# Kernel tuning notes

Hardware: AMD Instinct MI355X
Metric: run time of the kernel (lower is better)

## Reference

```python
import jax, jax.numpy as jnp
import numpy as np

B_SZ, L, D_MODEL = 2, 2048, 2048
INTER, HEADS, P, N, G, K = 4096, 64, 64, 128, 1, 4
CONV_DIM = INTER + 2 * G * N
EPS = 1e-5


def silu(x):
    return x * jax.nn.sigmoid(x)


def softplus_thresh(x, threshold=10.0):
    # matches source: where(x < thr, log(1+exp(x)), x)
    return jnp.where(x < threshold, jnp.log1p(jnp.exp(jnp.minimum(x, threshold))), x)


def setup_inputs() -> dict:
    key = jax.random.key(0)
    ks = jax.random.split(key, 8)
    s = 0.02
    return {
        "hidden_states": jax.random.normal(ks[0], (B_SZ, L, D_MODEL), jnp.float32),
        "W_z": jax.random.normal(ks[1], (D_MODEL, INTER), jnp.float32) * s,
        "W_xBC": jax.random.normal(ks[2], (D_MODEL, CONV_DIM), jnp.float32) * s,
        "W_dt": jax.random.normal(ks[3], (D_MODEL, HEADS), jnp.float32) * s,
        "conv_w": jax.random.normal(ks[4], (CONV_DIM, K), jnp.float32) * 0.1,
        "conv_b": jnp.zeros((CONV_DIM,), jnp.float32),
        "dt_bias": jax.random.uniform(ks[5], (HEADS,), jnp.float32, -2.0, 0.0),
        "A_log": jnp.log(jnp.arange(1, HEADS + 1, dtype=jnp.float32)),
        "D": jnp.ones((HEADS,), jnp.float32),
        "norm_w": jnp.ones((INTER,), jnp.float32),
        "W_out": jax.random.normal(ks[6], (INTER, D_MODEL), jnp.float32) * s,
    }


def reference(hidden_states, W_z, W_xBC, W_dt, conv_w, conv_b, dt_bias, A_log, D, norm_w, W_out):
    b, l, _ = hidden_states.shape
    Hg = HEADS // G  # heads per group

    gate = hidden_states @ W_z                      # [b,l,INTER]
    xBC = hidden_states @ W_xBC                     # [b,l,CONV_DIM]
    dt = softplus_thresh(hidden_states @ W_dt + dt_bias)  # [b,l,H]

    # causal depthwise conv1d + silu (padding=K-1, truncated to seq_len)
    xp = jnp.pad(xBC, ((0, 0), (K - 1, 0), (0, 0)))
    kern = jnp.transpose(conv_w)[:, None, :]        # [K,1,CONV_DIM] (WIO)
    xBC = jax.lax.conv_general_dilated(
        xp, kern, (1,), 'VALID',
        dimension_numbers=('NWC', 'WIO', 'NWC'),
        feature_group_count=CONV_DIM)
    xBC = silu(xBC + conv_b)

    gns = G * N
    x = xBC[..., :INTER].reshape(b, l, G, Hg, P)
    Bm = xBC[..., INTER:INTER + gns].reshape(b, l, G, N)
    Cm = xBC[..., INTER + gns:].reshape(b, l, G, N)

    A = -jnp.exp(A_log)                             # [H]
    dA = jnp.exp(dt * A).reshape(b, l, G, Hg)       # [b,l,G,Hg]
    dtx = dt.reshape(b, l, G, Hg)[..., None] * x    # [b,l,G,Hg,P]

    def step(state, inp):
        dA_t, dtx_t, B_t, C_t = inp
        # state: [b,G,Hg,P,N]
        state = state * dA_t[..., None, None] + dtx_t[..., None] * B_t[:, :, None, None, :]
        y_t = jnp.einsum('bghpn,bgn->bghp', state, C_t)
        return state, y_t

    xs = (jnp.moveaxis(dA, 1, 0), jnp.moveaxis(dtx, 1, 0),
          jnp.moveaxis(Bm, 1, 0), jnp.moveaxis(Cm, 1, 0))
    state0 = jnp.zeros((b, G, Hg, P, N), jnp.float32)
    _, ys = jax.lax.scan(step, state0, xs)          # [l,b,G,Hg,P]
    y = jnp.moveaxis(ys, 0, 1) + D.reshape(G, Hg)[..., None] * x
    scan_out = y.reshape(b, l, INTER)

    # gated RMSNorm within groups
    hs = scan_out.reshape(b, l, G, INTER // G).astype(jnp.float32)
    gt = gate.reshape(b, l, G, INTER // G).astype(jnp.float32)
    hs = hs * silu(gt)
    var = jnp.mean(hs * hs, axis=-1, keepdims=True)
    hs = hs * jax.lax.rsqrt(var + EPS)
    normed = norm_w * hs.reshape(b, l, INTER)

    return normed @ W_out
```

## Files before the change

kernel.cpp:

```cpp
#include <hip/hip_runtime.h>
#include <hip/hip_bf16.h>
#include <math.h>

typedef unsigned short u16;
typedef unsigned int   u32;
typedef __attribute__((ext_vector_type(8))) short short8;
typedef __attribute__((ext_vector_type(4))) float f32x4;

#define B_SZ     2
#define LSEQ     2048
#define DMODEL   2048
#define INTER    4096
#define HEADS    64
#define NSTATE   128
#define CONV_DIM 4352
#define XSTR     8576
#define NMAIN    8192
#define NTAILC   512
#define NTAILS   384
#define EPS      1e-5f
#define QCH      64
#define NCHUNK   (LSEQ / QCH)

__device__ __forceinline__ float bf2f(u16 u) {
    u32 v = ((u32)u) << 16;
    return __builtin_bit_cast(float, v);
}
__device__ __forceinline__ u16 f2bf(float x) {
    __hip_bfloat16 h = __float2bfloat16(x);
    return __builtin_bit_cast(u16, h);
}
__device__ __forceinline__ u32 pack2(float lo, float hi) {
    return (u32)f2bf(lo) | ((u32)f2bf(hi) << 16);
}
__device__ __forceinline__ void gl2lds16(const void* g, void* l) {
    __builtin_amdgcn_global_load_lds(
        (const __attribute__((address_space(1))) u32*)g,
        (__attribute__((address_space(3))) u32*)l, 16, 0, 0);
}

__global__ __launch_bounds__(256) void cvt_f32_bf16(
    const float* __restrict__ in, u16* __restrict__ out, int n4)
{
    int i = blockIdx.x * 256 + threadIdx.x;
    if (i >= n4) return;
    float4 v = ((const float4*)in)[i];
    ushort4 o;
    o.x = f2bf(v.x); o.y = f2bf(v.y); o.z = f2bf(v.z); o.w = f2bf(v.w);
    ((ushort4*)out)[i] = o;
}

__global__ __launch_bounds__(256) void tr_f32_bf16(
    const float* __restrict__ in, u16* __restrict__ out, int R, int C)
{
    __shared__ u16 tile[64][68];
    const int r0 = blockIdx.y * 64, c0 = blockIdx.x * 64;
    const int tr = threadIdx.x >> 4, tc = (threadIdx.x & 15) * 4;
    #pragma unroll
    for (int i = 0; i < 4; ++i) {
        int r = tr + i * 16;
        float4 v = *(const float4*)(in + (size_t)(r0 + r) * C + c0 + tc);
        tile[r][tc + 0] = f2bf(v.x);
        tile[r][tc + 1] = f2bf(v.y);
        tile[r][tc + 2] = f2bf(v.z);
        tile[r][tc + 3] = f2bf(v.w);
    }
    __syncthreads();
    #pragma unroll
    for (int i = 0; i < 4; ++i) {
        int oc = tr + i * 16;
        ushort4 o;
        o.x = tile[tc + 0][oc];
        o.y = tile[tc + 1][oc];
        o.z = tile[tc + 2][oc];
        o.w = tile[tc + 3][oc];
        *(ushort4*)(out + (size_t)(c0 + oc) * R + r0 + tc) = o;
    }
}

#define SA(c) (smem + (c) * 32768)
#define SB(c) (smem + (c) * 32768 + 16384)
#define STGA(c, q, ko) gl2lds16(gA + (size_t)((q) * 64) * lda + (ko), SA(c) + (q) * 4096 + lbase)
#define STGB(c, q, ko) gl2lds16(gB + (size_t)((q) * 64) * ldb + (ko), SB(c) + (q) * 4096 + lbase)

template<int OUT_BF16>
__global__ __launch_bounds__(512, 2) void gemm8(
    const u16* __restrict__ A, const u16* __restrict__ Bt, void* __restrict__ Co,
    int K, int lda, int ldb, int ldc, int Nstore)
{
    __shared__ __align__(16) u16 smem[65536];
    const int tid  = threadIdx.x;
    const int wave = tid >> 6, lane = tid & 63;
    const int wm = wave >> 2, wn = wave & 3;
    const int lr = lane & 15, lq = lane >> 4;

    const int nbx = gridDim.x;
    const int bid = blockIdx.y * nbx + blockIdx.x;
    const int nwg = nbx * gridDim.y;
    const int cpx = nwg >> 3;
    const int swz = (bid & 7) * cpx + (bid >> 3);
    const int n0 = (swz % nbx) * 256;
    const int m0 = (swz / nbx) * 256;
    const int kbase = blockIdx.z * K;

    const int srow  = tid >> 3;
    const int scb8  = ((tid & 7) ^ (srow & 7)) << 3;
    const int lbase = (tid >> 6) << 9;
    const u16* gA = A  + (size_t)(m0 + srow) * lda + kbase + scb8;
    const u16* gB = Bt + (size_t)(n0 + srow) * ldb + kbase + scb8;

    f32x4 acc[8][4];
    #pragma unroll
    for (int i = 0; i < 8; ++i)
        #pragma unroll
        for (int j = 0; j < 4; ++j) acc[i][j] = (f32x4)0.f;

    const int nt = K >> 6;

    STGA(0, 0, 0); STGA(0, 1, 0); STGA(0, 2, 0); STGA(0, 3, 0);
    STGB(0, 0, 0); STGB(0, 1, 0); STGB(0, 2, 0); STGB(0, 3, 0);
    __builtin_amdgcn_sched_barrier(0);
    asm volatile("s_waitcnt vmcnt(0)" ::: "memory");
    __builtin_amdgcn_s_barrier();

    for (int t = 0; t < nt; ++t) {
        const int c = t & 1;
        if (t + 1 < nt) {
            const int k1 = (t + 1) << 6;
            STGA(c ^ 1, 0, k1); STGA(c ^ 1, 1, k1);
            STGA(c ^ 1, 2, k1); STGA(c ^ 1, 3, k1);
            STGB(c ^ 1, 0, k1); STGB(c ^ 1, 1, k1);
            STGB(c ^ 1, 2, k1); STGB(c ^ 1, 3, k1);
        }
        __builtin_amdgcn_sched_barrier(0);
        const u16* Ab = SA(c);
        const u16* Bb = SB(c);
        #pragma unroll
        for (int kk = 0; kk < 2; ++kk) {
            short8 a8[8], b4[4];
            #pragma unroll
            for (int i = 0; i < 8; ++i)
                a8[i] = *(const short8*)(Ab + (wm * 128 + i * 16 + lr) * 64
                                         + ((((kk) * 4 + lq) ^ (lr & 7)) << 3));
            #pragma unroll
            for (int j = 0; j < 4; ++j)
                b4[j] = *(const short8*)(Bb + (wn * 64 + j * 16 + lr) * 64
                                         + ((((kk) * 4 + lq) ^ (lr & 7)) << 3));
            __builtin_amdgcn_s_setprio(1);
            #pragma unroll
            for (int i = 0; i < 8; ++i)
                #pragma unroll
                for (int j = 0; j < 4; ++j)
                    acc[i][j] = __builtin_amdgcn_mfma_f32_16x16x32_bf16(
                        a8[i], b4[j], acc[i][j], 0, 0, 0);
            __builtin_amdgcn_s_setprio(0);
        }
        if (t + 1 < nt) {
            asm volatile("s_waitcnt vmcnt(0)" ::: "memory");
            __builtin_amdgcn_s_barrier();
        }
    }

    const int odd = lr & 1;
    const bool wstore = (n0 + wn * 64) < Nstore;
    #pragma unroll
    for (int i = 0; i < 8; ++i)
        #pragma unroll
        for (int j = 0; j < 4; ++j) {
            float v0 = acc[i][j][0], v1 = acc[i][j][1];
            float v2 = acc[i][j][2], v3 = acc[i][j][3];
            float n0v = __shfl_xor(v0, 1), n1v = __shfl_xor(v1, 1);
            float n2v = __shfl_xor(v2, 1), n3v = __shfl_xor(v3, 1);
            int colb  = n0 + wn * 64 + j * 16 + (lr & ~1);
            int rbase = m0 + wm * 128 + i * 16 + lq * 4 + odd * 2;
            if (wstore) {
                if (OUT_BF16) {
                    u32 w0 = odd ? pack2(n2v, v2) : pack2(v0, n0v);
                    u32 w1 = odd ? pack2(n3v, v3) : pack2(v1, n1v);
                    *(u32*)((u16*)Co + (size_t)rbase * ldc + colb) = w0;
                    *(u32*)((u16*)Co + (size_t)(rbase + 1) * ldc + colb) = w1;
                } else {
                    float* Cf = (float*)Co + (size_t)blockIdx.z * 4096 * ldc;
                    float2 f0 = odd ? make_float2(n2v, v2) : make_float2(v0, n0v);
                    float2 f1 = odd ? make_float2(n3v, v3) : make_float2(v1, n1v);
                    *(float2*)(Cf + (size_t)rbase * ldc + colb) = f0;
                    *(float2*)(Cf + (size_t)(rbase + 1) * ldc + colb) = f1;
                }
            }
        }
}

__global__ __launch_bounds__(256) void tail_add(
    const float* __restrict__ Pt, u16* __restrict__ xall_)
{
    int i = blockIdx.x * 256 + threadIdx.x;
    int row = i / 96, cq = (i % 96) * 4;
    const float* p = Pt + (size_t)row * NTAILC + cq;
    const size_t zs = (size_t)4096 * NTAILC;
    float4 a = *(const float4*)(p);
    float4 b = *(const float4*)(p + zs);
    float4 c = *(const float4*)(p + 2 * zs);
    float4 d = *(const float4*)(p + 3 * zs);
    ushort4 o;
    o.x = f2bf(a.x + b.x + c.x + d.x);
    o.y = f2bf(a.y + b.y + c.y + d.y);
    o.z = f2bf(a.z + b.z + c.z + d.z);
    o.w = f2bf(a.w + b.w + c.w + d.w);
    *(ushort4*)(xall_ + (size_t)row * XSTR + NMAIN + cq) = o;
}

__global__ __launch_bounds__(256) void add2_f32(
    const float* __restrict__ a, const float* __restrict__ b,
    float* __restrict__ o, int n4)
{
    int i = blockIdx.x * 256 + threadIdx.x;
    if (i >= n4) return;
    float4 x = ((const float4*)a)[i];
    float4 y = ((const float4*)b)[i];
    x.x += y.x; x.y += y.y; x.z += y.z; x.w += y.w;
    ((float4*)o)[i] = x;
}

__global__ void dt_kernel(const u16* __restrict__ xall,
                          float* __restrict__ dtb,
                          const float* __restrict__ dt_bias, int n)
{
    int i = blockIdx.x * 256 + threadIdx.x;
    if (i >= n) return;
    int h = i & 63, row = i >> 6;
    float x = bf2f(xall[(size_t)row * XSTR + INTER + CONV_DIM + h]) + dt_bias[h];
    dtb[i] = (x < 10.f) ? log1pf(expf(x)) : x;
}

__global__ __launch_bounds__(256) void conv_kernel(
    const u16* __restrict__ xall, const float* __restrict__ cw,
    const float* __restrict__ cb, u16* __restrict__ xout)
{
    int c4 = blockIdx.x * 256 + threadIdx.x;
    if (c4 >= CONV_DIM / 4) return;
    int c  = c4 * 4;
    int bt = blockIdx.y;
    int t  = bt & (LSEQ - 1);
    const u16* xi = xall + (size_t)bt * XSTR + INTER + c;
    float4 w0 = *(const float4*)(cw + (size_t)(c + 0) * 4);
    float4 w1 = *(const float4*)(cw + (size_t)(c + 1) * 4);
    float4 w2 = *(const float4*)(cw + (size_t)(c + 2) * 4);
    float4 w3 = *(const float4*)(cw + (size_t)(c + 3) * 4);
    float4 bb = *(const float4*)(cb + c);
    float a0 = bb.x, a1 = bb.y, a2 = bb.z, a3 = bb.w;
    ushort4 x0 = *(const ushort4*)(xi);
    a0 = fmaf(bf2f(x0.x), w0.w, a0); a1 = fmaf(bf2f(x0.y), w1.w, a1);
    a2 = fmaf(bf2f(x0.z), w2.w, a2); a3 = fmaf(bf2f(x0.w), w3.w, a3);
    if (t >= 1) {
        ushort4 xm = *(const ushort4*)(xi - XSTR);
        a0 = fmaf(bf2f(xm.x), w0.z, a0); a1 = fmaf(bf2f(xm.y), w1.z, a1);
        a2 = fmaf(bf2f(xm.z), w2.z, a2); a3 = fmaf(bf2f(xm.w), w3.z, a3);
    }
    if (t >= 2) {
        ushort4 xm = *(const ushort4*)(xi - 2 * XSTR);
        a0 = fmaf(bf2f(xm.x), w0.y, a0); a1 = fmaf(bf2f(xm.y), w1.y, a1);
        a2 = fmaf(bf2f(xm.z), w2.y, a2); a3 = fmaf(bf2f(xm.w), w3.y, a3);
    }
    if (t >= 3) {
        ushort4 xm = *(const ushort4*)(xi - 3 * XSTR);
        a0 = fmaf(bf2f(xm.x), w0.x, a0); a1 = fmaf(bf2f(xm.y), w1.x, a1);
        a2 = fmaf(bf2f(xm.z), w2.x, a2); a3 = fmaf(bf2f(xm.w), w3.x, a3);
    }
    ushort4 o;
    o.x = f2bf(a0 / (1.f + expf(-a0)));
    o.y = f2bf(a1 / (1.f + expf(-a1)));
    o.z = f2bf(a2 / (1.f + expf(-a2)));
    o.w = f2bf(a3 / (1.f + expf(-a3)));
    *(ushort4*)(xout + (size_t)bt * CONV_DIM + c) = o;
}

__global__ __launch_bounds__(256) void ssd_chunk_state(
    const u16* __restrict__ xc, const float* __restrict__ dtb,
    const float* __restrict__ A_log,
    u16* __restrict__ Tg, float* __restrict__ decayQ)
{
    const int bid = blockIdx.x;
    const int b = bid >> 11, h = (bid >> 5) & 63, c = bid & 31;
    const int t0 = c * QCH;
    const int tid = threadIdx.x;
    const int wave = tid >> 6, lane = tid & 63;
    const int lr = lane & 15, lq = lane >> 4;

    __shared__ __align__(16) u16 BT[128][72];
    __shared__ __align__(16) u16 XwT[64][72];
    __shared__ float sclL[QCH];

    const u16* xg = xc + (size_t)b * LSEQ * CONV_DIM;

    if (tid < 64) {
        float dtv = dtb[((size_t)b * LSEQ + t0 + tid) * HEADS + h];
        float a = -dtv * expf(A_log[h]);
        float s = a;
        #pragma unroll
        for (int off = 1; off < 64; off <<= 1) {
            float o = __shfl_up(s, off, 64);
            if (tid >= off) s += o;
        }
        float cq = __shfl(s, 63, 64);
        sclL[tid] = dtv * expf(cq - s);
        if (tid == 0) decayQ[((b * 64 + h) << 5) + c] = expf(cq);
    }
    __syncthreads();

    #pragma unroll
    for (int r = 0; r < 16; ++r) {
        int idx = tid + 256 * r, j = idx >> 6, p = idx & 63;
        float v = bf2f(xg[(size_t)(t0 + j) * CONV_DIM + h * 64 + p]);
        XwT[p][j] = f2bf(v * sclL[j]);
    }
    #pragma unroll
    for (int r = 0; r < 32; ++r) {
        int idx = tid + 256 * r, j = idx >> 7, n = idx & 127;
        BT[n][j] = xg[(size_t)(t0 + j) * CONV_DIM + INTER + n];
    }
    __syncthreads();

    f32x4 acc[8];
    #pragma unroll
    for (int i = 0; i < 8; ++i) acc[i] = (f32x4)0.f;
    #pragma unroll
    for (int k0 = 0; k0 < QCH; k0 += 32) {
        short8 af = *(const short8*)&XwT[wave * 16 + lr][k0 + lq * 8];
        #pragma unroll
        for (int nt = 0; nt < 8; ++nt) {
            short8 bfr = *(const short8*)&BT[nt * 16 + lr][k0 + lq * 8];
            acc[nt] = __builtin_amdgcn_mfma_f32_16x16x32_bf16(af, bfr, acc[nt], 0, 0, 0);
        }
    }
    u16* To = Tg + ((((size_t)(b * 64 + h)) * NCHUNK + c) * 64) * 128;
    #pragma unroll
    for (int nt = 0; nt < 8; ++nt)
        #pragma unroll
        for (int r = 0; r < 4; ++r)
            To[(wave * 16 + lq * 4 + r) * 128 + nt * 16 + lr] = f2bf(acc[nt][r]);
}

__global__ __launch_bounds__(256) void ssd_state_scan(
    u16* __restrict__ Tg, const float* __restrict__ decayQ)
{
    const int bh = blockIdx.x >> 2, nq = blockIdx.x & 3;
    const int tid = threadIdx.x;
    const int p = tid >> 2, nb = nq * 32 + (tid & 3) * 8;
    float S[8];
    #pragma unroll
    for (int m = 0; m < 8; ++m) S[m] = 0.f;

    for (int c = 0; c < NCHUNK; ++c) {
        u16* base = Tg + ((((size_t)bh * NCHUNK + c) * 64 + p) * 128) + nb;
        uint4 tv = *(const uint4*)base;
        uint4 sv;
        sv.x = pack2(S[0], S[1]);
        sv.y = pack2(S[2], S[3]);
        sv.z = pack2(S[4], S[5]);
        sv.w = pack2(S[6], S[7]);
        *(uint4*)base = sv;
        float dq = decayQ[(bh << 5) + c];
        const u32* w = (const u32*)&tv;
        #pragma unroll
        for (int e = 0; e < 4; ++e) {
            S[e*2]     = fmaf(dq, S[e*2],     bf2f((u16)(w[e] & 0xffffu)));
            S[e*2 + 1] = fmaf(dq, S[e*2 + 1], bf2f((u16)(w[e] >> 16)));
        }
    }
}

__global__ __launch_bounds__(256) void ssd_output(
    const u16* __restrict__ xc, const float* __restrict__ dtb,
    const float* __restrict__ A_log, const float* __restrict__ Dvec,
    const u16* __restrict__ Sg,
    u16* __restrict__ y)
{
    const int bid = blockIdx.x;
    const int b = bid >> 11, h = (bid >> 5) & 63, c = bid & 31;
    const int t0 = c * QCH;
    const int tid = threadIdx.x;
    const int wave = tid >> 6, lane = tid & 63;
    const int lr = lane & 15, lq = lane >> 4;

    __shared__ __align__(16) u16 C_lds[64][136];
    __shared__ __align__(16) u16 B_lds[64][136];
    __shared__ __align__(16) u16 S_lds[64][136];
    __shared__ __align__(16) u16 P_lds[64][72];
    __shared__ __align__(16) u16 XT[64][72];
    __shared__ float cumL[QCH], dtsL[QCH], escL[QCH];

    const u16* xg = xc + (size_t)b * LSEQ * CONV_DIM;

    if (tid < 64) {
        float dtv = dtb[((size_t)b * LSEQ + t0 + tid) * HEADS + h];
        float a = -dtv * expf(A_log[h]);
        float s = a;
        #pragma unroll
        for (int off = 1; off < 64; off <<= 1) {
            float o = __shfl_up(s, off, 64);
            if (tid >= off) s += o;
        }
        cumL[tid] = s;
        dtsL[tid] = dtv;
        escL[tid] = expf(s);
    }
    #pragma unroll
    for (int r4 = 0; r4 < 4; ++r4) {
        int idx4 = tid + 256 * r4;
        int j = idx4 >> 4, c8 = (idx4 & 15) * 8;
        *(uint4*)&B_lds[j][c8] = *(const uint4*)(xg + (size_t)(t0 + j) * CONV_DIM + INTER + c8);
        *(uint4*)&C_lds[j][c8] = *(const uint4*)(xg + (size_t)(t0 + j) * CONV_DIM + INTER + NSTATE + c8);
        *(uint4*)&S_lds[j][c8] = *(const uint4*)(Sg + ((((size_t)(b * 64 + h)) * NCHUNK + c) * 64 + j) * 128 + c8);
    }
    #pragma unroll
    for (int r = 0; r < 16; ++r) {
        int idx = tid + 256 * r, j = idx >> 6, p = idx & 63;
        XT[p][j] = xg[(size_t)(t0 + j) * CONV_DIM + h * 64 + p];
    }
    __syncthreads();

    f32x4 accG[4];
    #pragma unroll
    for (int i = 0; i < 4; ++i) accG[i] = (f32x4)0.f;
    #pragma unroll
    for (int k0 = 0; k0 < NSTATE; k0 += 32) {
        short8 af = *(const short8*)&C_lds[wave * 16 + lr][k0 + lq * 8];
        #pragma unroll
        for (int jt = 0; jt < 4; ++jt) {
            short8 bfr = *(const short8*)&B_lds[jt * 16 + lr][k0 + lq * 8];
            accG[jt] = __builtin_amdgcn_mfma_f32_16x16x32_bf16(af, bfr, accG[jt], 0, 0, 0);
        }
    }
    #pragma unroll
    for (int jt = 0; jt < 4; ++jt)
        #pragma unroll
        for (int r = 0; r < 4; ++r) {
            int ii = wave * 16 + lq * 4 + r;
            int jj = jt * 16 + lr;
            float v = (jj <= ii)
                ? accG[jt][r] * dtsL[jj] * expf(cumL[ii] - cumL[jj]) : 0.f;
            P_lds[ii][jj] = f2bf(v);
        }
    __syncthreads();

    f32x4 accY[4], accZ[4];
    #pragma unroll
    for (int i = 0; i < 4; ++i) { accY[i] = (f32x4)0.f; accZ[i] = (f32x4)0.f; }
    #pragma unroll
    for (int k0 = 0; k0 < QCH; k0 += 32) {
        short8 af = *(const short8*)&P_lds[wave * 16 + lr][k0 + lq * 8];
        #pragma unroll
        for (int pt = 0; pt < 4; ++pt) {
            short8 bfr = *(const short8*)&XT[pt * 16 + lr][k0 + lq * 8];
            accY[pt] = __builtin_amdgcn_mfma_f32_16x16x32_bf16(af, bfr, accY[pt], 0, 0, 0);
        }
    }
    #pragma unroll
    for (int k0 = 0; k0 < NSTATE; k0 += 32) {
        short8 af = *(const short8*)&C_lds[wave * 16 + lr][k0 + lq * 8];
        #pragma unroll
        for (int pt = 0; pt < 4; ++pt) {
            short8 bfr = *(const short8*)&S_lds[pt * 16 + lr][k0 + lq * 8];
            accZ[pt] = __builtin_amdgcn_mfma_f32_16x16x32_bf16(af, bfr, accZ[pt], 0, 0, 0);
        }
    }

    const float Dh = Dvec[h];
    u16* yg = y + ((size_t)b * LSEQ + t0) * XSTR + h * 64;
    #pragma unroll
    for (int pt = 0; pt < 4; ++pt)
        #pragma unroll
        for (int r = 0; r < 4; ++r) {
            int ii = wave * 16 + lq * 4 + r;
            int pp = pt * 16 + lr;
            float xv = bf2f(XT[pp][ii]);
            float o = accY[pt][r] + escL[ii] * accZ[pt][r] + Dh * xv;
            yg[(size_t)ii * XSTR + pp] = f2bf(o);
        }
}

__global__ __launch_bounds__(256) void norm_kernel(
    u16* __restrict__ xall, const float* __restrict__ w)
{
    const int row = blockIdx.x;
    const u16* yr = xall + (size_t)row * XSTR + INTER;
    u16*       gr = xall + (size_t)row * XSTR;
    const int tid = threadIdx.x;

    float v[16];
    float ss = 0.f;
    #pragma unroll
    for (int i = 0; i < 2; ++i) {
        int e0 = i * 2048 + tid * 8;
        uint4 hv4 = *(const uint4*)(yr + e0);
        uint4 gv4 = *(const uint4*)(gr + e0);
        const u16* hp = (const u16*)&hv4;
        const u16* gp = (const u16*)&gv4;
        #pragma unroll
        for (int k = 0; k < 8; ++k) {
            float hv = bf2f(hp[k]);
            float g  = bf2f(gp[k]);
            float val = hv * (g / (1.f + expf(-g)));
            v[i * 8 + k] = val;
            ss = fmaf(val, val, ss);
        }
    }
    #pragma unroll
    for (int o = 32; o > 0; o >>= 1) ss += __shfl_xor(ss, o);
    __shared__ float part[4];
    if ((tid & 63) == 0) part[tid >> 6] = ss;
    __syncthreads();
    float tot  = part[0] + part[1] + part[2] + part[3];
    float rinv = rsqrtf(tot * (1.f / INTER) + EPS);
    #pragma unroll
    for (int i = 0; i < 2; ++i) {
        int e0 = i * 2048 + tid * 8;
        float4 wa = *(const float4*)(w + e0);
        float4 wb = *(const float4*)(w + e0 + 4);
        uint4 sv;
        sv.x = pack2(wa.x * v[i*8+0] * rinv, wa.y * v[i*8+1] * rinv);
        sv.y = pack2(wa.z * v[i*8+2] * rinv, wa.w * v[i*8+3] * rinv);
        sv.z = pack2(wb.x * v[i*8+4] * rinv, wb.y * v[i*8+5] * rinv);
        sv.w = pack2(wb.z * v[i*8+6] * rinv, wb.w * v[i*8+7] * rinv);
        *(uint4*)(gr + e0) = sv;
    }
}

extern "C" void kernel_launch(void* const* d_in, const int* in_sizes, int n_in,
                              void* d_out, int out_size, void* d_ws, size_t ws_size,
                              hipStream_t stream)
{
    const float* hs      = (const float*)d_in[0];
    const float* W_z     = (const float*)d_in[1];
    const float* W_xBC   = (const float*)d_in[2];
    const float* W_dt    = (const float*)d_in[3];
    const float* conv_w  = (const float*)d_in[4];
    const float* conv_b  = (const float*)d_in[5];
    const float* dt_bias = (const float*)d_in[6];
    const float* A_log   = (const float*)d_in[7];
    const float* Dv      = (const float*)d_in[8];
    const float* norm_w  = (const float*)d_in[9];
    const float* W_out   = (const float*)d_in[10];
    float* out = (float*)d_out;
    char*  w8  = (char*)d_ws;

    u16* hs_bf  = (u16*)(w8 + 0);
    u16* Wt_all = (u16*)(w8 + 16777216);
    u16* Tbuf   = (u16*)(w8 + 0);
    float* Cpart= (float*)(w8 + 0);
    u16* Wt_out = (u16*)(w8 + 67108864);
    u16* xall   = (u16*)(w8 + 83886080);
    u16* xconv  = (u16*)(w8 + 154140672);
    float* Ptail= (float*)(w8 + 154140672);
    float* dtb  = (float*)(w8 + 189792256);
    float* dcq  = (float*)(w8 + 190840832);

    const int M = B_SZ * LSEQ;

    cvt_f32_bf16<<<(M * DMODEL / 4 + 255) / 256, 256, 0, stream>>>(hs, hs_bf, M * DMODEL / 4);
    tr_f32_bf16<<<dim3(INTER / 64,    DMODEL / 64), 256, 0, stream>>>(W_z,   Wt_all, DMODEL, INTER);
    tr_f32_bf16<<<dim3(CONV_DIM / 64, DMODEL / 64), 256, 0, stream>>>(W_xBC, Wt_all + (size_t)INTER * DMODEL, DMODEL, CONV_DIM);
    tr_f32_bf16<<<dim3(1,             DMODEL / 64), 256, 0, stream>>>(W_dt,  Wt_all + (size_t)(INTER + CONV_DIM) * DMODEL, DMODEL, 64);
    hipMemsetAsync(Wt_all + (size_t)(INTER + CONV_DIM + 64) * DMODEL, 0, (size_t)192 * DMODEL * 2, stream);
    tr_f32_bf16<<<dim3(DMODEL / 64,   INTER / 64),  256, 0, stream>>>(W_out, Wt_out, INTER, DMODEL);

    gemm8<1><<<dim3(NMAIN / 256, M / 256, 1), 512, 0, stream>>>(
        hs_bf, Wt_all, (void*)xall, DMODEL , DMODEL, DMODEL,
        XSTR , NMAIN );
    gemm8<0><<<dim3(NTAILC / 256, M / 256, 4), 512, 0, stream>>>(
        hs_bf, Wt_all + (size_t)NMAIN * DMODEL, (void*)Ptail, DMODEL / 4 ,
        DMODEL, DMODEL, NTAILC , NTAILS );
    tail_add<<<M * (NTAILS / 4) / 256, 256, 0, stream>>>(Ptail, xall);

    dt_kernel<<<(M * HEADS + 255) / 256, 256, 0, stream>>>(xall, dtb, dt_bias, M * HEADS);
    conv_kernel<<<dim3((CONV_DIM / 4 + 255) / 256, M), 256, 0, stream>>>(xall, conv_w, conv_b, xconv);

    ssd_chunk_state<<<B_SZ * HEADS * NCHUNK, 256, 0, stream>>>(xconv, dtb, A_log, Tbuf, dcq);
    ssd_state_scan<<<B_SZ * HEADS * 4, 256, 0, stream>>>(Tbuf, dcq);
    ssd_output<<<B_SZ * HEADS * NCHUNK, 256, 0, stream>>>(xconv, dtb, A_log, Dv, Tbuf, xall + INTER);

    norm_kernel<<<M, 256, 0, stream>>>(xall, norm_w);

    gemm8<0><<<dim3(DMODEL / 256, M / 256, 2), 512, 0, stream>>>(
        xall, Wt_out, (void*)Cpart, INTER / 2 , XSTR ,
        INTER , DMODEL , DMODEL );
    add2_f32<<<(M * DMODEL / 4 + 255) / 256, 256, 0, stream>>>(
        Cpart, Cpart + (size_t)M * DMODEL, out, M * DMODEL / 4);
}
```

Before: 624.0 us.

## Widen GEMM tiles to 256x512 with K=32 stages and 3-way split-K output

The GEMM kernel moves from a 256x256 tile with K-step 64 to a 256x512 tile with K-step 32. Each wave now holds an 8x8 grid of MFMA accumulators, and A fragments are software-prefetched inside the inner loop. The goal is more MFMA work per LDS byte and fewer blocks for the input projection. The output projection switches from 2-way to 3-way split-K (slices of 1376) so more blocks fill the CUs, and a 3-input add reduces the partial sums. In exchange the kernel needs many more accumulator registers, which risks spills or lower occupancy, and the split-K reduction adds an extra fp32 partial buffer to read.

```diff
diff --git a/kernel.cpp b/kernel.cpp
--- a/kernel.cpp
+++ b/kernel.cpp
@@ -78,17 +78,16 @@
     }
 }
 
-#define SA(c) (smem + (c) * 32768)
-#define SB(c) (smem + (c) * 32768 + 16384)
-#define STGA(c, q, ko) gl2lds16(gA + (size_t)((q) * 64) * lda + (ko), SA(c) + (q) * 4096 + lbase)
-#define STGB(c, q, ko) gl2lds16(gB + (size_t)((q) * 64) * ldb + (ko), SB(c) + (q) * 4096 + lbase)
+#define SA(c) (smem + (c) * 24576)
+#define SB(c) (smem + (c) * 24576 + 8192)
 
 template<int OUT_BF16>
-__global__ __launch_bounds__(512, 2) void gemm8(
-    const u16* __restrict__ A, const u16* __restrict__ Bt, void* __restrict__ Co,
-    int K, int lda, int ldb, int ldc, int Nstore)
-{
-    __shared__ __align__(16) u16 smem[65536];
+__global__ __launch_bounds__(512, 2) void gemmw(
+    const u16* __restrict__ A, const u16* __restrict__ Bt,
+    void* __restrict__ Co, void* __restrict__ Co2, int Z2,
+    int K, int Kslice, int lda, int ldb, int ldc, int Nstore)
+{
+    __shared__ __align__(16) u16 smem[49152];
     const int tid  = threadIdx.x;
     const int wave = tid >> 6, lane = tid & 63;
     const int wm = wave >> 2, wn = wave & 3;
@@ -99,62 +98,67 @@
     const int nwg = nbx * gridDim.y;
     const int cpx = nwg >> 3;
     const int swz = (bid & 7) * cpx + (bid >> 3);
-    const int n0 = (swz % nbx) * 256;
+    const int n0 = (swz % nbx) * 512;
     const int m0 = (swz / nbx) * 256;
-    const int kbase = blockIdx.z * K;
-
-    const int srow  = tid >> 3;
-    const int scb8  = ((tid & 7) ^ (srow & 7)) << 3;
-    const int lbase = (tid >> 6) << 9;
-    const u16* gA = A  + (size_t)(m0 + srow) * lda + kbase + scb8;
-    const u16* gB = Bt + (size_t)(n0 + srow) * ldb + kbase + scb8;
-
-    f32x4 acc[8][4];
+    const int kbase = blockIdx.z * Kslice;
+    const int kthis = (Kslice < K - kbase) ? Kslice : (K - kbase);
+    const int nt = kthis >> 5;
+
+    const int scb8  = (((tid & 3) ^ ((tid >> 3) & 3)) << 3);
+    const int lbase = wave << 9;
+    const u16* gA = A  + (size_t)(m0 + (tid >> 2)) * lda + kbase + scb8;
+    const u16* gB = Bt + (size_t)(n0 + (tid >> 2)) * ldb + kbase + scb8;
+
+    f32x4 acc[8][8];
     #pragma unroll
     for (int i = 0; i < 8; ++i)
         #pragma unroll
-        for (int j = 0; j < 4; ++j) acc[i][j] = (f32x4)0.f;
-
-    const int nt = K >> 6;
-
-    STGA(0, 0, 0); STGA(0, 1, 0); STGA(0, 2, 0); STGA(0, 3, 0);
-    STGB(0, 0, 0); STGB(0, 1, 0); STGB(0, 2, 0); STGB(0, 3, 0);
+        for (int j = 0; j < 8; ++j) acc[i][j] = (f32x4)0.f;
+
+    gl2lds16(gA,                      SA(0) + lbase);
+    gl2lds16(gA + (size_t)128 * lda,  SA(0) + 4096 + lbase);
+    #pragma unroll
+    for (int q = 0; q < 4; ++q)
+        gl2lds16(gB + (size_t)(q * 128) * ldb, SB(0) + q * 4096 + lbase);
     __builtin_amdgcn_sched_barrier(0);
     asm volatile("s_waitcnt vmcnt(0)" ::: "memory");
     __builtin_amdgcn_s_barrier();
 
+    const int sws = ((lq ^ ((lr >> 1) & 3)) << 3);
+
     for (int t = 0; t < nt; ++t) {
         const int c = t & 1;
         if (t + 1 < nt) {
-            const int k1 = (t + 1) << 6;
-            STGA(c ^ 1, 0, k1); STGA(c ^ 1, 1, k1);
-            STGA(c ^ 1, 2, k1); STGA(c ^ 1, 3, k1);
-            STGB(c ^ 1, 0, k1); STGB(c ^ 1, 1, k1);
-            STGB(c ^ 1, 2, k1); STGB(c ^ 1, 3, k1);
+            const int k1 = (t + 1) << 5;
+            gl2lds16(gA + k1,                     SA(c ^ 1) + lbase);
+            gl2lds16(gA + (size_t)128 * lda + k1, SA(c ^ 1) + 4096 + lbase);
+            #pragma unroll
+            for (int q = 0; q < 4; ++q)
+                gl2lds16(gB + (size_t)(q * 128) * ldb + k1, SB(c ^ 1) + q * 4096 + lbase);
         }
         __builtin_amdgcn_sched_barrier(0);
+
         const u16* Ab = SA(c);
         const u16* Bb = SB(c);
-        #pragma unroll
-        for (int kk = 0; kk < 2; ++kk) {
-            short8 a8[8], b4[4];
+        short8 b8[8];
+        short8 ac = *(const short8*)(Ab + (wm * 128 + lr) * 32 + sws);
+        #pragma unroll
+        for (int j = 0; j < 8; ++j)
+            b8[j] = *(const short8*)(Bb + (wn * 128 + j * 16 + lr) * 32 + sws);
+        __builtin_amdgcn_s_setprio(1);
+        #pragma unroll
+        for (int i = 0; i < 8; ++i) {
+            short8 an = ac;
+            if (i < 7)
+                an = *(const short8*)(Ab + (wm * 128 + (i + 1) * 16 + lr) * 32 + sws);
             #pragma unroll
-            for (int i = 0; i < 8; ++i)
-                a8[i] = *(const short8*)(Ab + (wm * 128 + i * 16 + lr) * 64
-                                         + ((((kk) * 4 + lq) ^ (lr & 7)) << 3));
-            #pragma unroll
-            for (int j = 0; j < 4; ++j)
-                b4[j] = *(const short8*)(Bb + (wn * 64 + j * 16 + lr) * 64
-                                         + ((((kk) * 4 + lq) ^ (lr & 7)) << 3));
-            __builtin_amdgcn_s_setprio(1);
-            #pragma unroll
-            for (int i = 0; i < 8; ++i)
-                #pragma unroll
-                for (int j = 0; j < 4; ++j)
-                    acc[i][j] = __builtin_amdgcn_mfma_f32_16x16x32_bf16(
-                        a8[i], b4[j], acc[i][j], 0, 0, 0);
-            __builtin_amdgcn_s_setprio(0);
-        }
+            for (int j = 0; j < 8; ++j)
+                acc[i][j] = __builtin_amdgcn_mfma_f32_16x16x32_bf16(
+                    ac, b8[j], acc[i][j], 0, 0, 0);
+            ac = an;
+        }
+        __builtin_amdgcn_s_setprio(0);
+        __builtin_amdgcn_sched_barrier(0);
         if (t + 1 < nt) {
             asm volatile("s_waitcnt vmcnt(0)" ::: "memory");
             __builtin_amdgcn_s_barrier();
@@ -162,25 +166,26 @@
     }
 
     const int odd = lr & 1;
-    const bool wstore = (n0 + wn * 64) < Nstore;
+    float* Cf = (blockIdx.z < (unsigned)Z2)
+        ? ((float*)Co  + (size_t)blockIdx.z * 4096 * ldc)
+        : ((float*)Co2 + (size_t)(blockIdx.z - Z2) * 4096 * ldc);
     #pragma unroll
     for (int i = 0; i < 8; ++i)
         #pragma unroll
-        for (int j = 0; j < 4; ++j) {
+        for (int j = 0; j < 8; ++j) {
             float v0 = acc[i][j][0], v1 = acc[i][j][1];
             float v2 = acc[i][j][2], v3 = acc[i][j][3];
             float n0v = __shfl_xor(v0, 1), n1v = __shfl_xor(v1, 1);
             float n2v = __shfl_xor(v2, 1), n3v = __shfl_xor(v3, 1);
-            int colb  = n0 + wn * 64 + j * 16 + (lr & ~1);
+            int colb  = n0 + wn * 128 + j * 16 + (lr & ~1);
             int rbase = m0 + wm * 128 + i * 16 + lq * 4 + odd * 2;
-            if (wstore) {
+            if ((n0 + wn * 128 + j * 16) < Nstore) {
                 if (OUT_BF16) {
                     u32 w0 = odd ? pack2(n2v, v2) : pack2(v0, n0v);
                     u32 w1 = odd ? pack2(n3v, v3) : pack2(v1, n1v);
                     *(u32*)((u16*)Co + (size_t)rbase * ldc + colb) = w0;
                     *(u32*)((u16*)Co + (size_t)(rbase + 1) * ldc + colb) = w1;
                 } else {
-                    float* Cf = (float*)Co + (size_t)blockIdx.z * 4096 * ldc;
                     float2 f0 = odd ? make_float2(n2v, v2) : make_float2(v0, n0v);
                     float2 f1 = odd ? make_float2(n3v, v3) : make_float2(v1, n1v);
                     *(float2*)(Cf + (size_t)rbase * ldc + colb) = f0;
@@ -209,15 +214,16 @@
     *(ushort4*)(xall_ + (size_t)row * XSTR + NMAIN + cq) = o;
 }
 
-__global__ __launch_bounds__(256) void add2_f32(
+__global__ __launch_bounds__(256) void add3_f32(
     const float* __restrict__ a, const float* __restrict__ b,
-    float* __restrict__ o, int n4)
+    const float* __restrict__ c, float* __restrict__ o, int n4)
 {
     int i = blockIdx.x * 256 + threadIdx.x;
     if (i >= n4) return;
     float4 x = ((const float4*)a)[i];
     float4 y = ((const float4*)b)[i];
-    x.x += y.x; x.y += y.y; x.z += y.z; x.w += y.w;
+    float4 z = ((const float4*)c)[i];
+    x.x += y.x + z.x; x.y += y.y + z.y; x.z += y.z + z.z; x.w += y.w + z.w;
     ((float4*)o)[i] = x;
 }
 
@@ -547,11 +553,12 @@
     u16* hs_bf  = (u16*)(w8 + 0);
     u16* Wt_all = (u16*)(w8 + 16777216);
     u16* Tbuf   = (u16*)(w8 + 0);
-    float* Cpart= (float*)(w8 + 0);
+    float* Cp01 = (float*)(w8 + 0);
     u16* Wt_out = (u16*)(w8 + 67108864);
     u16* xall   = (u16*)(w8 + 83886080);
     u16* xconv  = (u16*)(w8 + 154140672);
     float* Ptail= (float*)(w8 + 154140672);
+    float* Cp2  = (float*)(w8 + 154140672);
     float* dtb  = (float*)(w8 + 189792256);
     float* dcq  = (float*)(w8 + 190840832);
 
@@ -564,12 +571,12 @@
     hipMemsetAsync(Wt_all + (size_t)(INTER + CONV_DIM + 64) * DMODEL, 0, (size_t)192 * DMODEL * 2, stream);
     tr_f32_bf16<<<dim3(DMODEL / 64,   INTER / 64),  256, 0, stream>>>(W_out, Wt_out, INTER, DMODEL);
 
-    gemm8<1><<<dim3(NMAIN / 256, M / 256, 1), 512, 0, stream>>>(
-        hs_bf, Wt_all, (void*)xall, DMODEL , DMODEL, DMODEL,
-        XSTR , NMAIN );
-    gemm8<0><<<dim3(NTAILC / 256, M / 256, 4), 512, 0, stream>>>(
-        hs_bf, Wt_all + (size_t)NMAIN * DMODEL, (void*)Ptail, DMODEL / 4 ,
-        DMODEL, DMODEL, NTAILC , NTAILS );
+    gemmw<1><<<dim3(NMAIN / 512, M / 256, 1), 512, 0, stream>>>(
+        hs_bf, Wt_all, (void*)xall, nullptr, 8,
+        DMODEL , DMODEL , DMODEL, DMODEL, XSTR , NMAIN);
+    gemmw<0><<<dim3(1, M / 256, 4), 512, 0, stream>>>(
+        hs_bf, Wt_all + (size_t)NMAIN * DMODEL, (void*)Ptail, nullptr, 8,
+        DMODEL , DMODEL / 4 , DMODEL, DMODEL, NTAILC , NTAILS);
     tail_add<<<M * (NTAILS / 4) / 256, 256, 0, stream>>>(Ptail, xall);
 
     dt_kernel<<<(M * HEADS + 255) / 256, 256, 0, stream>>>(xall, dtb, dt_bias, M * HEADS);
@@ -581,9 +588,10 @@
 
     norm_kernel<<<M, 256, 0, stream>>>(xall, norm_w);
 
-    gemm8<0><<<dim3(DMODEL / 256, M / 256, 2), 512, 0, stream>>>(
-        xall, Wt_out, (void*)Cpart, INTER / 2 , XSTR ,
-        INTER , DMODEL , DMODEL );
-    add2_f32<<<(M * DMODEL / 4 + 255) / 256, 256, 0, stream>>>(
-        Cpart, Cpart + (size_t)M * DMODEL, out, M * DMODEL / 4);
-}
+    gemmw<0><<<dim3(DMODEL / 512, M / 256, 3), 512, 0, stream>>>(
+        xall, Wt_out, (void*)Cp01, (void*)Cp2, 2,
+        INTER , 1376 , XSTR , INTER ,
+        DMODEL , DMODEL);
+    add3_f32<<<(M * DMODEL / 4 + 255) / 256, 256, 0, stream>>>(
+        Cp01, Cp01 + (size_t)M * DMODEL, Cp2, out, M * DMODEL / 4);
+}
```

After: 1.523 ms. 144% more time.
